# Kernel optimization log

Hardware: AMD Instinct MI355X
Metric: run time of the kernel (lower is better)

## Reference

```python
import jax, jax.numpy as jnp
import numpy as np

B = 512          # batch
SIZE_IN = 1024   # input features
SIZE_OUT = 256   # output features
NUM_Q = 16       # quantiles


def setup_inputs() -> dict:
    key = jax.random.key(0)
    k1, k2, k3, k4 = jax.random.split(key, 4)
    x = jax.random.normal(k1, (B, SIZE_IN), dtype=jnp.float32)
    indices = jax.random.randint(k2, (B, SIZE_IN), 0, NUM_Q, dtype=jnp.int64)
    # param_index table: row (q*SIZE_IN + j) holds a SIZE_OUT weight vector
    param_table = jax.random.normal(k3, (NUM_Q * SIZE_IN, SIZE_OUT), dtype=jnp.float32)
    bias = jax.random.normal(k4, (SIZE_OUT,), dtype=jnp.float32)
    return {"x": x, "indices": indices, "param_table": param_table, "bias": bias}


def reference(x, indices, param_table, bias):
    size_in = x.shape[1]
    # flat row index into the quantile-indexed table: q*size_in + feature_pos
    flat_idx = indices * size_in + jnp.arange(size_in, dtype=indices.dtype)[None, :]  # [B, In]
    gathered = param_table[flat_idx]  # [B, In, Out] gather
    # scale each gathered weight vector by the scalar input and reduce over features
    out = jnp.einsum('bi,bio->bo', x, gathered)  # [B, Out]
    return out + bias
```

## Files before the change

### kernel.cpp

```cpp
#include <hip/hip_runtime.h>


constexpr int BATCH    = 512;
constexpr int SIZE_IN  = 1024;
constexpr int SIZE_OUT = 256;

constexpr int THREADS    = 256;
constexpr int WAVES      = THREADS / 64;
constexpr int I_PER_WAVE = SIZE_IN / WAVES;

__global__ __launch_bounds__(THREADS, 2)
void indexed_linear_kernel(const float* __restrict__ x,
                           const int*   __restrict__ idx,
                           const float* __restrict__ table,
                           const float* __restrict__ bias,
                           float*       __restrict__ out)
{
    __shared__ int2  xr[SIZE_IN];
    __shared__ float red[WAVES][SIZE_OUT];

    const int b    = blockIdx.x;
    const int tid  = threadIdx.x;
    const int wave = tid >> 6;
    const int lane = tid & 63;

    {
        const float4 xv = reinterpret_cast<const float4*>(x   + b * SIZE_IN)[tid];
        const int4   qv = reinterpret_cast<const int4*>(idx + b * SIZE_IN)[tid];
        const int ibase = tid * 4;
        xr[ibase + 0] = make_int2(__float_as_int(xv.x), (qv.x * SIZE_IN + ibase + 0) * SIZE_OUT);
        xr[ibase + 1] = make_int2(__float_as_int(xv.y), (qv.y * SIZE_IN + ibase + 1) * SIZE_OUT);
        xr[ibase + 2] = make_int2(__float_as_int(xv.z), (qv.z * SIZE_IN + ibase + 2) * SIZE_OUT);
        xr[ibase + 3] = make_int2(__float_as_int(xv.w), (qv.w * SIZE_IN + ibase + 3) * SIZE_OUT);
    }
    __syncthreads();

    float4 acc = make_float4(0.f, 0.f, 0.f, 0.f);
    const int j0    = wave * I_PER_WAVE;
    const int olane = lane * 4;

    #pragma unroll 8
    for (int j = 0; j < I_PER_WAVE; ++j) {
        const int2  p  = xr[j0 + j];
        const float xj = __int_as_float(p.x);
        const float4 w = *reinterpret_cast<const float4*>(table + p.y + olane);
        acc.x = fmaf(xj, w.x, acc.x);
        acc.y = fmaf(xj, w.y, acc.y);
        acc.z = fmaf(xj, w.z, acc.z);
        acc.w = fmaf(xj, w.w, acc.w);
    }

    *reinterpret_cast<float4*>(&red[wave][olane]) = acc;
    __syncthreads();

    float s = bias[tid];
    #pragma unroll
    for (int w = 0; w < WAVES; ++w) s += red[w][tid];
    out[b * SIZE_OUT + tid] = s;
}

extern "C" void kernel_launch(void* const* d_in, const int* in_sizes, int n_in,
                              void* d_out, int out_size, void* d_ws, size_t ws_size,
                              hipStream_t stream) {
    const float* x     = (const float*)d_in[0];
    const int*   idx   = (const int*)d_in[1];
    const float* table = (const float*)d_in[2];
    const float* bias  = (const float*)d_in[3];
    float*       out   = (float*)d_out;

    indexed_linear_kernel<<<dim3(BATCH), dim3(THREADS), 0, stream>>>(x, idx, table, bias, out);
}
```

Before: 90.32 us.

## Recast quantile gather as one-hot bf16 MFMA GEMM with split-Q reduction

Replaces the per-row gather-and-FMA kernel with a four-kernel pipeline. The first kernel expands x into per-quantile masked bf16 matrices. The second transposes and converts the table to bf16. The third runs a 16x16x32 bf16 MFMA GEMM per quantile, and the fourth sums the 16 partial outputs and adds bias. The aim is to turn the latency-bound scattered gather into dense matrix-core work, at the cost of about 33MB of workspace traffic, extra launches and bf16 rounding of both x and the weights. If the workspace is too small, a simpler and slower gather kernel runs instead.

```diff
diff --git a/kernel.cpp b/kernel.cpp
--- a/kernel.cpp
+++ b/kernel.cpp
@@ -1,61 +1,182 @@
 #include <hip/hip_runtime.h>
-
-
-constexpr int BATCH    = 512;
+#include <stdint.h>
+
+
 constexpr int SIZE_IN  = 1024;
 constexpr int SIZE_OUT = 256;
-
-constexpr int THREADS    = 256;
-constexpr int WAVES      = THREADS / 64;
-constexpr int I_PER_WAVE = SIZE_IN / WAVES;
-
-__global__ __launch_bounds__(THREADS, 2)
-void indexed_linear_kernel(const float* __restrict__ x,
-                           const int*   __restrict__ idx,
-                           const float* __restrict__ table,
-                           const float* __restrict__ bias,
-                           float*       __restrict__ out)
-{
-    __shared__ int2  xr[SIZE_IN];
-    __shared__ float red[WAVES][SIZE_OUT];
-
-    const int b    = blockIdx.x;
-    const int tid  = threadIdx.x;
-    const int wave = tid >> 6;
-    const int lane = tid & 63;
-
+constexpr int BATCH    = 512;
+constexpr int NUM_Q    = 16;
+constexpr int KTOT     = NUM_Q * SIZE_IN;
+constexpr int A_LD     = 1040;
+constexpr int TM       = 32;
+
+constexpr size_t A_OFF    = 0;
+constexpr size_t A_BYTES  = (size_t)NUM_Q * BATCH * A_LD * 2;
+constexpr size_t BT_OFF   = A_OFF + A_BYTES;
+constexpr size_t BT_BYTES = (size_t)SIZE_OUT * KTOT * 2;
+constexpr size_t P_OFF    = BT_OFF + BT_BYTES;
+constexpr size_t P_BYTES  = (size_t)NUM_Q * BATCH * SIZE_OUT * 4;
+constexpr size_t WS_NEED  = P_OFF + P_BYTES;
+
+typedef short short8   __attribute__((ext_vector_type(8)));
+typedef float floatx4  __attribute__((ext_vector_type(4)));
+
+__device__ inline uint32_t pack2bf(float lo, float hi) {
+    uint32_t a = __float_as_uint(lo) + 0x8000u;
+    uint32_t b = __float_as_uint(hi) + 0x8000u;
+    return __builtin_amdgcn_perm(b, a, 0x07060302);
+}
+__device__ inline uint16_t bf1(float f) {
+    return (uint16_t)((__float_as_uint(f) + 0x8000u) >> 16);
+}
+
+__global__ __launch_bounds__(256)
+void expand_a(const float* __restrict__ x, const int* __restrict__ idx,
+              uint16_t* __restrict__ A)
+{
+    const int g  = blockIdx.x * 256 + threadIdx.x;
+    const int b  = g >> 7;
+    const int i0 = (g & 127) * 8;
+    const float4 xv0 = *(const float4*)(x + b * SIZE_IN + i0);
+    const float4 xv1 = *(const float4*)(x + b * SIZE_IN + i0 + 4);
+    const int4   iv0 = *(const int4*)(idx + b * SIZE_IN + i0);
+    const int4   iv1 = *(const int4*)(idx + b * SIZE_IN + i0 + 4);
+    const float xs[8] = {xv0.x,xv0.y,xv0.z,xv0.w, xv1.x,xv1.y,xv1.z,xv1.w};
+    const int   is[8] = {iv0.x,iv0.y,iv0.z,iv0.w, iv1.x,iv1.y,iv1.z,iv1.w};
+    #pragma unroll
+    for (int q = 0; q < NUM_Q; ++q) {
+        float m[8];
+        #pragma unroll
+        for (int j = 0; j < 8; ++j) m[j] = (is[j] == q) ? xs[j] : 0.f;
+        uint4 d;
+        d.x = pack2bf(m[0], m[1]); d.y = pack2bf(m[2], m[3]);
+        d.z = pack2bf(m[4], m[5]); d.w = pack2bf(m[6], m[7]);
+        *(uint4*)(A + (size_t)(q * BATCH + b) * A_LD + i0) = d;
+    }
+}
+
+__global__ __launch_bounds__(256)
+void transpose_bt(const float* __restrict__ table, uint16_t* __restrict__ Bt)
+{
+    __shared__ uint16_t t[64][72];
+    const int k0  = (blockIdx.x & 255) * 64;
+    const int o0  = (blockIdx.x >> 8) * 64;
+    const int tid = threadIdx.x;
     {
-        const float4 xv = reinterpret_cast<const float4*>(x   + b * SIZE_IN)[tid];
-        const int4   qv = reinterpret_cast<const int4*>(idx + b * SIZE_IN)[tid];
-        const int ibase = tid * 4;
-        xr[ibase + 0] = make_int2(__float_as_int(xv.x), (qv.x * SIZE_IN + ibase + 0) * SIZE_OUT);
-        xr[ibase + 1] = make_int2(__float_as_int(xv.y), (qv.y * SIZE_IN + ibase + 1) * SIZE_OUT);
-        xr[ibase + 2] = make_int2(__float_as_int(xv.z), (qv.z * SIZE_IN + ibase + 2) * SIZE_OUT);
-        xr[ibase + 3] = make_int2(__float_as_int(xv.w), (qv.w * SIZE_IN + ibase + 3) * SIZE_OUT);
+        const int kr = tid >> 4;
+        const int oc = (tid & 15) * 4;
+        #pragma unroll
+        for (int rr = 0; rr < 4; ++rr) {
+            const int k = rr * 16 + kr;
+            const float4 v = *(const float4*)(table + (size_t)(k0 + k) * SIZE_OUT + o0 + oc);
+            t[oc + 0][k] = bf1(v.x);
+            t[oc + 1][k] = bf1(v.y);
+            t[oc + 2][k] = bf1(v.z);
+            t[oc + 3][k] = bf1(v.w);
+        }
     }
     __syncthreads();
-
-    float4 acc = make_float4(0.f, 0.f, 0.f, 0.f);
-    const int j0    = wave * I_PER_WAVE;
-    const int olane = lane * 4;
+    const int orow = tid >> 2;
+    const int kc   = (tid & 3) * 16;
+    const uint4 lo = *(const uint4*)(&t[orow][kc]);
+    const uint4 hi = *(const uint4*)(&t[orow][kc + 8]);
+    uint16_t* dst = Bt + (size_t)(o0 + orow) * KTOT + k0 + kc;
+    *(uint4*)dst       = lo;
+    *(uint4*)(dst + 8) = hi;
+}
+
+__global__ __launch_bounds__(512, 1)
+void gemm_splitq(const uint16_t* __restrict__ A,
+                 const uint16_t* __restrict__ Bt,
+                 float* __restrict__ parts)
+{
+    __shared__ uint16_t Al[TM * A_LD];
+    const int tid   = threadIdx.x;
+    const int q     = blockIdx.x & 15;
+    const int bt    = blockIdx.x >> 4;
+    const int b0    = bt * TM;
+    const int w     = tid >> 6;
+    const int lane  = tid & 63;
+    const int nlane = lane & 15;
+    const int quad  = lane >> 4;
+
+    {
+        const uint4* src = (const uint4*)(A + (size_t)(q * BATCH + b0) * A_LD);
+        uint4* dst = (uint4*)Al;
+        #pragma unroll
+        for (int c = 0; c < 8; ++c)
+            dst[c * 512 + tid] = src[c * 512 + tid];
+        if (tid < 64) dst[8 * 512 + tid] = src[8 * 512 + tid];
+    }
+    __syncthreads();
+
+    const uint16_t* bp0 = Bt + (size_t)(w * 32 + nlane) * KTOT + q * SIZE_IN + quad * 8;
+    const uint16_t* bp1 = bp0 + (size_t)16 * KTOT;
+    const uint16_t* ar0 = Al + nlane * A_LD + quad * 8;
+    const uint16_t* ar1 = ar0 + 16 * A_LD;
+
+    floatx4 acc00 = {0,0,0,0}, acc01 = {0,0,0,0}, acc10 = {0,0,0,0}, acc11 = {0,0,0,0};
 
     #pragma unroll 8
-    for (int j = 0; j < I_PER_WAVE; ++j) {
-        const int2  p  = xr[j0 + j];
-        const float xj = __int_as_float(p.x);
-        const float4 w = *reinterpret_cast<const float4*>(table + p.y + olane);
-        acc.x = fmaf(xj, w.x, acc.x);
-        acc.y = fmaf(xj, w.y, acc.y);
-        acc.z = fmaf(xj, w.z, acc.z);
-        acc.w = fmaf(xj, w.w, acc.w);
-    }
-
-    *reinterpret_cast<float4*>(&red[wave][olane]) = acc;
+    for (int kb = 0; kb < 32; ++kb) {
+        const short8 a0 = *(const short8*)(ar0 + kb * 32);
+        const short8 a1 = *(const short8*)(ar1 + kb * 32);
+        const short8 bq0 = *(const short8*)(bp0 + kb * 32);
+        const short8 bq1 = *(const short8*)(bp1 + kb * 32);
+        acc00 = __builtin_amdgcn_mfma_f32_16x16x32_bf16(a0, bq0, acc00, 0, 0, 0);
+        acc10 = __builtin_amdgcn_mfma_f32_16x16x32_bf16(a1, bq0, acc10, 0, 0, 0);
+        acc01 = __builtin_amdgcn_mfma_f32_16x16x32_bf16(a0, bq1, acc01, 0, 0, 0);
+        acc11 = __builtin_amdgcn_mfma_f32_16x16x32_bf16(a1, bq1, acc11, 0, 0, 0);
+    }
+
+    float* pq = parts + ((size_t)q * BATCH + b0) * SIZE_OUT;
+    const int col0 = w * 32 + nlane;
+    #pragma unroll
+    for (int rr = 0; rr < 4; ++rr) {
+        const int r0 = quad * 4 + rr;
+        pq[(size_t)r0 * SIZE_OUT + col0]            = acc00[rr];
+        pq[(size_t)r0 * SIZE_OUT + col0 + 16]       = acc01[rr];
+        pq[(size_t)(r0 + 16) * SIZE_OUT + col0]     = acc10[rr];
+        pq[(size_t)(r0 + 16) * SIZE_OUT + col0 + 16]= acc11[rr];
+    }
+}
+
+__global__ __launch_bounds__(256)
+void reduce_ws(const float* __restrict__ ws, const float* __restrict__ bias,
+               float* __restrict__ out)
+{
+    const int e  = blockIdx.x * 256 + threadIdx.x;
+    const int o4 = e & 63;
+    const float4* w4 = reinterpret_cast<const float4*>(ws);
+    float4 s = reinterpret_cast<const float4*>(bias)[o4];
+    #pragma unroll
+    for (int q = 0; q < NUM_Q; ++q) {
+        const float4 v = w4[(size_t)q * (BATCH * SIZE_OUT / 4) + e];
+        s.x += v.x; s.y += v.y; s.z += v.z; s.w += v.w;
+    }
+    reinterpret_cast<float4*>(out)[e] = s;
+}
+
+__global__ __launch_bounds__(256)
+void fallback_gather(const float* __restrict__ x, const int* __restrict__ idx,
+                     const float* __restrict__ table, const float* __restrict__ bias,
+                     float* __restrict__ out)
+{
+    __shared__ int2 xr[SIZE_IN];
+    const int b = blockIdx.x, tid = threadIdx.x;
+    const float4 xv = reinterpret_cast<const float4*>(x + b * SIZE_IN)[tid];
+    const int4   qv = reinterpret_cast<const int4*>(idx + b * SIZE_IN)[tid];
+    const int ib = tid * 4;
+    xr[ib+0] = make_int2(__float_as_int(xv.x), (qv.x*SIZE_IN+ib+0)*SIZE_OUT);
+    xr[ib+1] = make_int2(__float_as_int(xv.y), (qv.y*SIZE_IN+ib+1)*SIZE_OUT);
+    xr[ib+2] = make_int2(__float_as_int(xv.z), (qv.z*SIZE_IN+ib+2)*SIZE_OUT);
+    xr[ib+3] = make_int2(__float_as_int(xv.w), (qv.w*SIZE_IN+ib+3)*SIZE_OUT);
     __syncthreads();
-
     float s = bias[tid];
-    #pragma unroll
-    for (int w = 0; w < WAVES; ++w) s += red[w][tid];
+    for (int j = 0; j < SIZE_IN; ++j) {
+        const int2 p = xr[j];
+        s = fmaf(__int_as_float(p.x), table[p.y + tid], s);
+    }
     out[b * SIZE_OUT + tid] = s;
 }
 
@@ -68,5 +189,15 @@
     const float* bias  = (const float*)d_in[3];
     float*       out   = (float*)d_out;
 
-    indexed_linear_kernel<<<dim3(BATCH), dim3(THREADS), 0, stream>>>(x, idx, table, bias, out);
-}
+    if (ws_size >= WS_NEED) {
+        uint16_t* Aws = (uint16_t*)((char*)d_ws + A_OFF);
+        uint16_t* Btw = (uint16_t*)((char*)d_ws + BT_OFF);
+        float*    pts = (float*)((char*)d_ws + P_OFF);
+        expand_a    <<<dim3(BATCH * 128 / 256), dim3(256), 0, stream>>>(x, idx, Aws);
+        transpose_bt<<<dim3((KTOT / 64) * (SIZE_OUT / 64)), dim3(256), 0, stream>>>(table, Btw);
+        gemm_splitq <<<dim3((BATCH / TM) * NUM_Q), dim3(512), 0, stream>>>(Aws, Btw, pts);
+        reduce_ws   <<<dim3(BATCH * SIZE_OUT / 4 / 256), dim3(256), 0, stream>>>(pts, bias, out);
+    } else {
+        fallback_gather<<<dim3(BATCH), dim3(256), 0, stream>>>(x, idx, table, bias, out);
+    }
+}
```

New measurement: 100.7 us. +11.5%, slower.
